# Performance work log

Measured on AMD Instinct MI355X. Metric: run time of the kernel, lower is better.

The kernel has to match this reference:

```python
import jax, jax.numpy as jnp
import numpy as np

B, S, D, H = 4, 2048, 1024, 16
HD = D // H  # head_dim = 64


def setup_inputs() -> dict:
    key = jax.random.key(0)
    ks = jax.random.split(key, 5)
    s = 1.0 / np.sqrt(D)
    return {
        "x": jax.random.normal(ks[0], (B, S, D), jnp.float32),
        "Wq": jax.random.normal(ks[1], (D, D), jnp.float32) * s,
        "Wk": jax.random.normal(ks[2], (D, D), jnp.float32) * s,
        "Wv": jax.random.normal(ks[3], (D, D), jnp.float32) * s,
        "Wo": jax.random.normal(ks[4], (D, D), jnp.float32) * s,
        "bo": jnp.zeros((D,), jnp.float32),
    }


def reference(x, Wq, Wk, Wv, Wo, bo):
    b, s, d = x.shape
    # projections (torch Linear: x @ W.T; weights here stored as [in, out] equivalent)
    q = (x @ Wq).reshape(b, s, H, HD).transpose(0, 2, 1, 3)  # [b,h,s,hd]
    k = (x @ Wk).reshape(b, s, H, HD).transpose(0, 2, 1, 3)
    v = (x @ Wv).reshape(b, s, H, HD).transpose(0, 2, 1, 3)
    scores = jnp.einsum("bhqd,bhkd->bhqk", q, k) * (HD ** -0.5)
    causal = jnp.tril(jnp.ones((s, s), bool))  # mask==0 -> -inf
    scores = jnp.where(causal, scores, -jnp.inf)
    attn = jax.nn.softmax(scores, axis=-1)
    out = jnp.einsum("bhqk,bhkd->bhqd", attn, v)
    out = out.transpose(0, 2, 1, 3).reshape(b, s, d)
    return out @ Wo + bo
```

## Files before the change

kernel.cpp:

```cpp
#include <hip/hip_runtime.h>
#include <cstdint>
#include <cstddef>

typedef __attribute__((ext_vector_type(8))) short bf16x8;
typedef __attribute__((ext_vector_type(4))) short bf16x4;
typedef __attribute__((ext_vector_type(4))) float f32x4;

constexpr int Bsz = 4, Ssz = 2048, Dsz = 1024, Hn = 16, HDsz = 64;
constexpr int Msz = Bsz * Ssz;
constexpr float LOG2E = 1.4426950408889634f;

#define MFMA16(a, b, c) __builtin_amdgcn_mfma_f32_16x16x16bf16_1k(a, b, c, 0, 0, 0)
#define MFMA32(a, b, c) __builtin_amdgcn_mfma_f32_16x16x32_bf16(a, b, c, 0, 0, 0)

__device__ __forceinline__ unsigned short f2bf(float f) {
  union { float f; unsigned int u; } v; v.f = f;
  unsigned int r = v.u + 0x7fffu + ((v.u >> 16) & 1u);
  return (unsigned short)(r >> 16);
}

typedef __attribute__((address_space(1))) const unsigned int gu32;
typedef __attribute__((address_space(3))) unsigned int lu32;
__device__ __forceinline__ void async_cp16(const unsigned short* g, unsigned short* l) {
  __builtin_amdgcn_global_load_lds((gu32*)g, (lu32*)l, 16, 0, 0);
}

__global__ void prep_kernel(const float* __restrict__ x, unsigned short* __restrict__ xb,
                            const float* __restrict__ W0, const float* __restrict__ W1,
                            const float* __restrict__ W2, const float* __restrict__ W3,
                            unsigned short* __restrict__ T0, unsigned short* __restrict__ T1,
                            unsigned short* __restrict__ T2, unsigned short* __restrict__ T3) {
  const int z = blockIdx.z;
  if (z == 4) {
    const int i0 = (blockIdx.y * 32 + blockIdx.x) * 2048 + threadIdx.x;
#pragma unroll
    for (int j = 0; j < 8; j++) {
      const int i = i0 + j * 256;
      const float4 v = reinterpret_cast<const float4*>(x)[i];
      ushort4 o;
      o.x = f2bf(v.x); o.y = f2bf(v.y); o.z = f2bf(v.z); o.w = f2bf(v.w);
      reinterpret_cast<ushort4*>(xb)[i] = o;
    }
    return;
  }
  __shared__ float tile[32][33];
  const float* W = (z == 0) ? W0 : (z == 1) ? W1 : (z == 2) ? W2 : W3;
  unsigned short* Wt = (z == 0) ? T0 : (z == 1) ? T1 : (z == 2) ? T2 : T3;
  int tx = threadIdx.x & 31, ty = threadIdx.x >> 5;
  int bx = blockIdx.x, by = blockIdx.y;
#pragma unroll
  for (int i = 0; i < 4; i++) {
    int k = by * 32 + ty + i * 8;
    tile[ty + i * 8][tx] = W[k * Dsz + bx * 32 + tx];
  }
  __syncthreads();
#pragma unroll
  for (int i = 0; i < 4; i++) {
    int nrow = bx * 32 + ty + i * 8;
    Wt[nrow * Dsz + by * 32 + tx] = f2bf(tile[tx][ty + i * 8]);
  }
}

enum { EPI_QKV = 0, EPI_OUT = 1 };

template <int EPI>
__global__ __launch_bounds__(512, 4)
void gemm_bk64(const unsigned short* __restrict__ A,
               const unsigned short* __restrict__ Bt,
               unsigned short* __restrict__ Qh,
               unsigned short* __restrict__ Kh,
               unsigned short* __restrict__ Vth,
               float* __restrict__ Out,
               const float* __restrict__ bias) {
  __shared__ unsigned short As[128 * 64];
  __shared__ unsigned short Bs[128 * 64];

  const int tid = threadIdx.x;
  const int w = tid >> 6, lane = tid & 63;
  const int l15 = lane & 15, quad = lane >> 4;
  const int wr = w >> 1, wc = w & 1;
  const int orig = blockIdx.y * gridDim.x + blockIdx.x;
  const int xcd = orig & 7, idx = orig >> 3;
  const int bm = (xcd << 3) | (idx & 7);
  const int bn = idx >> 3;
  const int rr = lane >> 3;
  const int scoff = ((lane & 7) ^ rr) * 8;

  f32x4 acc[2][4];
#pragma unroll
  for (int i = 0; i < 2; i++)
#pragma unroll
    for (int j = 0; j < 4; j++) acc[i][j] = (f32x4){0.f, 0.f, 0.f, 0.f};

  const int rowA0 = bm * 128, rowB0 = bn * 128;

  for (int kt = 0; kt < Dsz / 64; kt++) {
#pragma unroll
    for (int i = 0; i < 2; i++) {
      const int r8 = w * 16 + i * 8;
      async_cp16(&A[(size_t)(rowA0 + r8 + rr) * Dsz + kt * 64 + scoff], &As[r8 * 64]);
      async_cp16(&Bt[(size_t)(rowB0 + r8 + rr) * Dsz + kt * 64 + scoff], &Bs[r8 * 64]);
    }
    __syncthreads();

#pragma unroll
    for (int ks = 0; ks < 2; ks++) {
      bf16x8 af[2], bfr[4];
#pragma unroll
      for (int t = 0; t < 2; t++) {
        const int ra = wr * 32 + t * 16 + l15;
        af[t] = *reinterpret_cast<const bf16x8*>(
            &As[ra * 64 + (((ks * 4 + quad) ^ (ra & 7)) * 8)]);
      }
#pragma unroll
      for (int t = 0; t < 4; t++) {
        const int rb = wc * 64 + t * 16 + l15;
        bfr[t] = *reinterpret_cast<const bf16x8*>(
            &Bs[rb * 64 + (((ks * 4 + quad) ^ (rb & 7)) * 8)]);
      }
#pragma unroll
      for (int i = 0; i < 2; i++)
#pragma unroll
        for (int j = 0; j < 4; j++)
          acc[i][j] = MFMA32(af[i], bfr[j], acc[i][j]);
    }
    __syncthreads();
  }

  if (EPI == EPI_QKV) {
    const int proj = (bn * 128) >> 10;
#pragma unroll
    for (int i = 0; i < 2; i++) {
#pragma unroll
      for (int j = 0; j < 4; j++) {
        const int n = bn * 128 + wc * 64 + j * 16 + l15;
        const int nn = n & 1023, h = nn >> 6, hd = nn & 63;
        const int m0 = bm * 128 + wr * 32 + i * 16 + quad * 4;
        const int b = m0 >> 11, s0 = m0 & (Ssz - 1);
        if (proj == 0) {
#pragma unroll
          for (int r = 0; r < 4; r++)
            Qh[((size_t)(b * Hn + h) * Ssz + s0 + r) * HDsz + hd] =
                f2bf(acc[i][j][r] * (0.125f * LOG2E));
        } else if (proj == 1) {
#pragma unroll
          for (int r = 0; r < 4; r++)
            Kh[((size_t)(b * Hn + h) * Ssz + s0 + r) * HDsz + hd] = f2bf(acc[i][j][r]);
        } else {
          ushort4 o;
          o.x = f2bf(acc[i][j][0]); o.y = f2bf(acc[i][j][1]);
          o.z = f2bf(acc[i][j][2]); o.w = f2bf(acc[i][j][3]);
          *reinterpret_cast<ushort4*>(
              &Vth[((size_t)(b * Hn + h) * HDsz + hd) * Ssz + s0]) = o;
        }
      }
    }
  } else {
#pragma unroll
    for (int i = 0; i < 2; i++) {
#pragma unroll
      for (int j = 0; j < 4; j++) {
        const int n = bn * 128 + wc * 64 + j * 16 + l15;
        const int m0 = bm * 128 + wr * 32 + i * 16 + quad * 4;
#pragma unroll
        for (int r = 0; r < 4; r++)
          Out[(size_t)(m0 + r) * Dsz + n] = acc[i][j][r] + bias[n];
      }
    }
  }
}

__global__ __launch_bounds__(256, 4)
void flash_kernel(const unsigned short* __restrict__ Q,
                  const unsigned short* __restrict__ Kg,
                  const unsigned short* __restrict__ Vt,
                  unsigned short* __restrict__ AO) {
  __shared__ unsigned short Ks[64 * 64];
  __shared__ unsigned short Vs[64 * 64];

  const int tid = threadIdx.x;
  const int w = tid >> 6, lane = tid & 63;
  const int l15 = lane & 15, quad = lane >> 4;
  const int rr = lane >> 3;

  const int linear = blockIdx.y * 16 + blockIdx.x;
  const int bh = (linear & 7) * 8 + ((linear >> 3) & 7);
  const int g = linear >> 6, gk = g >> 2, ga = g & 3;
  const int t = (gk == 0) ? 15 - ga : (gk == 1) ? 8 + ga : (gk == 2) ? 7 - ga : ga;

  const unsigned short* Qb = Q + (size_t)bh * Ssz * HDsz;
  const unsigned short* Kb = Kg + (size_t)bh * Ssz * HDsz;
  const unsigned short* Vb = Vt + (size_t)bh * HDsz * Ssz;
  const int b = bh / Hn, h = bh % Hn;

  const int hl = (l15 & 7) ^ ((l15 >> 3) << 2);

  const int q0 = t * 128;
  const int rowStart = q0 + w * 32;

  bf16x8 qf[2][2];
#pragma unroll
  for (int tm = 0; tm < 2; tm++)
#pragma unroll
    for (int ks = 0; ks < 2; ks++)
      qf[tm][ks] = *reinterpret_cast<const bf16x8*>(
          &Qb[(size_t)(rowStart + tm * 16 + l15) * HDsz + ks * 32 + quad * 8]);

  f32x4 oacc[2][4];
  float lpart[2] = {0.f, 0.f};
#pragma unroll
  for (int tm = 0; tm < 2; tm++)
#pragma unroll
    for (int tn = 0; tn < 4; tn++) oacc[tm][tn] = (f32x4){0.f, 0.f, 0.f, 0.f};

  const int nkb = 2 * t + 2;
  for (int kb = 0; kb < nkb; kb++) {
    const int kv0 = kb * 64;
#pragma unroll
    for (int i = 0; i < 2; i++) {
      const int r8 = w * 16 + i * 8;
      const int sc = (((lane & 7) ^ rr ^ (i << 2))) * 8;
      async_cp16(&Kb[(size_t)(kv0 + r8 + rr) * HDsz + sc], &Ks[r8 * 64]);
      async_cp16(&Vb[(size_t)(r8 + rr) * Ssz + kv0 + sc], &Vs[r8 * 64]);
    }
    __syncthreads();

    const bool skip = (kv0 >= rowStart + 32);
    if (!skip) {
      f32x4 sc[4][2];
#pragma unroll
      for (int tn = 0; tn < 4; tn++)
#pragma unroll
        for (int tm = 0; tm < 2; tm++) sc[tn][tm] = (f32x4){0.f, 0.f, 0.f, 0.f};
#pragma unroll
      for (int ks = 0; ks < 2; ks++) {
#pragma unroll
        for (int tn = 0; tn < 4; tn++) {
          const int rk = tn * 16 + l15;
          bf16x8 kf = *reinterpret_cast<const bf16x8*>(
              &Ks[rk * 64 + (((ks * 4 + quad) ^ hl) * 8)]);
#pragma unroll
          for (int tm = 0; tm < 2; tm++)
            sc[tn][tm] = MFMA32(kf, qf[tm][ks], sc[tn][tm]);
        }
      }

      const bool needMask = (kv0 + 63 > rowStart);
      if (needMask) {
#pragma unroll
        for (int tn = 0; tn < 4; tn++)
#pragma unroll
          for (int tm = 0; tm < 2; tm++) {
            const int qrow = rowStart + tm * 16 + l15;
#pragma unroll
            for (int r = 0; r < 4; r++)
              if (kv0 + tn * 16 + quad * 4 + r > qrow) sc[tn][tm][r] = -1e30f;
          }
      }

      unsigned int pk[4][2][2];
#pragma unroll
      for (int tn = 0; tn < 4; tn++)
#pragma unroll
        for (int tm = 0; tm < 2; tm++) {
          union { float f; unsigned int u; } e0, e1, e2, e3;
          e0.f = __builtin_amdgcn_exp2f(sc[tn][tm][0]);
          e1.f = __builtin_amdgcn_exp2f(sc[tn][tm][1]);
          e2.f = __builtin_amdgcn_exp2f(sc[tn][tm][2]);
          e3.f = __builtin_amdgcn_exp2f(sc[tn][tm][3]);
          lpart[tm] += (e0.f + e1.f) + (e2.f + e3.f);
          pk[tn][tm][0] = __builtin_amdgcn_perm(e1.u, e0.u, 0x07060302u);
          pk[tn][tm][1] = __builtin_amdgcn_perm(e3.u, e2.u, 0x07060302u);
        }

#pragma unroll
      for (int tn = 0; tn < 4; tn++) {
        bf16x4 pa[2];
#pragma unroll
        for (int tm = 0; tm < 2; tm++) {
          union { unsigned int u[2]; bf16x4 v; } cv;
          cv.u[0] = pk[tn][tm][0]; cv.u[1] = pk[tn][tm][1];
          pa[tm] = cv.v;
        }
#pragma unroll
        for (int to = 0; to < 4; to++) {
          const int rv = to * 16 + l15;
          const int chunk = tn * 2 + (quad >> 1);
          bf16x4 vf = *reinterpret_cast<const bf16x4*>(
              (const char*)Vs + rv * 128 + ((chunk ^ hl) * 16) + (quad & 1) * 8);
#pragma unroll
          for (int tm = 0; tm < 2; tm++)
            oacc[tm][to] = MFMA16(pa[tm], vf, oacc[tm][to]);
        }
      }
    }
    __syncthreads();
  }

#pragma unroll
  for (int tm = 0; tm < 2; tm++) {
    float lf = lpart[tm];
    lf += __shfl_xor(lf, 16);
    lf += __shfl_xor(lf, 32);
    float linv[4];
#pragma unroll
    for (int r = 0; r < 4; r++) {
      union { float f; int i; } cv;
      cv.f = lf;
      cv.i = __builtin_amdgcn_ds_bpermute((quad * 4 + r) * 4, cv.i);
      linv[r] = 1.f / cv.f;
    }
#pragma unroll
    for (int r = 0; r < 4; r++) {
      const int s = rowStart + tm * 16 + quad * 4 + r;
      const size_t m = (size_t)b * Ssz + s;
#pragma unroll
      for (int tn = 0; tn < 4; tn++) {
        const int n = h * HDsz + tn * 16 + l15;
        AO[m * Dsz + n] = f2bf(oacc[tm][tn][r] * linv[r]);
      }
    }
  }
}

extern "C" void kernel_launch(void* const* d_in, const int* in_sizes, int n_in,
                              void* d_out, int out_size, void* d_ws, size_t ws_size,
                              hipStream_t stream) {
  const float* x  = (const float*)d_in[0];
  const float* Wq = (const float*)d_in[1];
  const float* Wk = (const float*)d_in[2];
  const float* Wv = (const float*)d_in[3];
  const float* Wo = (const float*)d_in[4];
  const float* bo = (const float*)d_in[5];
  float* out = (float*)d_out;

  unsigned short* xb  = (unsigned short*)d_ws;
  unsigned short* Wqt = xb + (size_t)Msz * Dsz;
  unsigned short* Wkt = Wqt + (size_t)Dsz * Dsz;
  unsigned short* Wvt = Wkt + (size_t)Dsz * Dsz;
  unsigned short* Wot = Wvt + (size_t)Dsz * Dsz;
  unsigned short* Qh  = Wot + (size_t)Dsz * Dsz;
  unsigned short* Kh  = Qh + (size_t)Msz * Dsz;
  unsigned short* Vth = Kh + (size_t)Msz * Dsz;
  unsigned short* AO  = Vth + (size_t)Msz * Dsz;

  prep_kernel<<<dim3(32, 32, 5), 256, 0, stream>>>(
      x, xb, Wq, Wk, Wv, Wo, Wqt, Wkt, Wvt, Wot);

  gemm_bk64<EPI_QKV><<<dim3(3 * Dsz / 128, Msz / 128), 512, 0, stream>>>(
      xb, Wqt, Qh, Kh, Vth, nullptr, nullptr);

  flash_kernel<<<dim3(16, Bsz * Hn), 256, 0, stream>>>(Qh, Kh, Vth, AO);

  gemm_bk64<EPI_OUT><<<dim3(Dsz / 128, Msz / 128), 512, 0, stream>>>(
      AO, Wot, nullptr, nullptr, nullptr, out, bo);
}
```

Measured before the change: 225.3 us.

## Halve flash attention query tile to 64 rows and double the grid

The flash kernel now gives each block 64 query rows (16 per wave) instead of 128, launches twice as many blocks, and raises the launch-bounds occupancy hint to 8 blocks per CU. The causal tile schedule is remapped so heavy and light tiles interleave across the 32 query tiles. The aim is more parallelism and a better causal load balance with fewer registers per thread. In exchange, each K/V tile loaded into LDS is reused by half as many query rows, so global and LDS traffic per FLOP roughly doubles.

```diff
diff --git a/kernel.cpp b/kernel.cpp
--- a/kernel.cpp
+++ b/kernel.cpp
@@ -170,7 +170,7 @@
   }
 }
 
-__global__ __launch_bounds__(256, 4)
+__global__ __launch_bounds__(256, 8)
 void flash_kernel(const unsigned short* __restrict__ Q,
                   const unsigned short* __restrict__ Kg,
                   const unsigned short* __restrict__ Vt,
@@ -185,8 +185,9 @@
 
   const int linear = blockIdx.y * 16 + blockIdx.x;
   const int bh = (linear & 7) * 8 + ((linear >> 3) & 7);
-  const int g = linear >> 6, gk = g >> 2, ga = g & 3;
-  const int t = (gk == 0) ? 15 - ga : (gk == 1) ? 8 + ga : (gk == 2) ? 7 - ga : ga;
+  const int g = linear >> 6;
+  const int gk = g >> 2, gr = g & 3;
+  const int t = (gk < 4) ? (gr * 8 + gk) : (31 - (gr * 8 + (gk - 4)));
 
   const unsigned short* Qb = Q + (size_t)bh * Ssz * HDsz;
   const unsigned short* Kb = Kg + (size_t)bh * Ssz * HDsz;
@@ -195,25 +196,21 @@
 
   const int hl = (l15 & 7) ^ ((l15 >> 3) << 2);
 
-  const int q0 = t * 128;
-  const int rowStart = q0 + w * 32;
-
-  bf16x8 qf[2][2];
-#pragma unroll
-  for (int tm = 0; tm < 2; tm++)
-#pragma unroll
-    for (int ks = 0; ks < 2; ks++)
-      qf[tm][ks] = *reinterpret_cast<const bf16x8*>(
-          &Qb[(size_t)(rowStart + tm * 16 + l15) * HDsz + ks * 32 + quad * 8]);
-
-  f32x4 oacc[2][4];
-  float lpart[2] = {0.f, 0.f};
-#pragma unroll
-  for (int tm = 0; tm < 2; tm++)
-#pragma unroll
-    for (int tn = 0; tn < 4; tn++) oacc[tm][tn] = (f32x4){0.f, 0.f, 0.f, 0.f};
-
-  const int nkb = 2 * t + 2;
+  const int q0 = t * 64;
+  const int rowStart = q0 + w * 16;
+
+  bf16x8 qf[2];
+#pragma unroll
+  for (int ks = 0; ks < 2; ks++)
+    qf[ks] = *reinterpret_cast<const bf16x8*>(
+        &Qb[(size_t)(rowStart + l15) * HDsz + ks * 32 + quad * 8]);
+
+  f32x4 oacc[4];
+  float lpart = 0.f;
+#pragma unroll
+  for (int to = 0; to < 4; to++) oacc[to] = (f32x4){0.f, 0.f, 0.f, 0.f};
+
+  const int nkb = t + 1;
   for (int kb = 0; kb < nkb; kb++) {
     const int kv0 = kb * 64;
 #pragma unroll
@@ -225,100 +222,79 @@
     }
     __syncthreads();
 
-    const bool skip = (kv0 >= rowStart + 32);
-    if (!skip) {
-      f32x4 sc[4][2];
+    f32x4 sc[4];
+#pragma unroll
+    for (int tn = 0; tn < 4; tn++) sc[tn] = (f32x4){0.f, 0.f, 0.f, 0.f};
+#pragma unroll
+    for (int ks = 0; ks < 2; ks++) {
+#pragma unroll
+      for (int tn = 0; tn < 4; tn++) {
+        const int rk = tn * 16 + l15;
+        bf16x8 kf = *reinterpret_cast<const bf16x8*>(
+            &Ks[rk * 64 + (((ks * 4 + quad) ^ hl) * 8)]);
+        sc[tn] = MFMA32(kf, qf[ks], sc[tn]);
+      }
+    }
+
+    const bool needMask = (kv0 + 63 > rowStart);
+    if (needMask) {
+      const int qrow = rowStart + l15;
 #pragma unroll
       for (int tn = 0; tn < 4; tn++)
 #pragma unroll
-        for (int tm = 0; tm < 2; tm++) sc[tn][tm] = (f32x4){0.f, 0.f, 0.f, 0.f};
-#pragma unroll
-      for (int ks = 0; ks < 2; ks++) {
-#pragma unroll
-        for (int tn = 0; tn < 4; tn++) {
-          const int rk = tn * 16 + l15;
-          bf16x8 kf = *reinterpret_cast<const bf16x8*>(
-              &Ks[rk * 64 + (((ks * 4 + quad) ^ hl) * 8)]);
-#pragma unroll
-          for (int tm = 0; tm < 2; tm++)
-            sc[tn][tm] = MFMA32(kf, qf[tm][ks], sc[tn][tm]);
-        }
-      }
-
-      const bool needMask = (kv0 + 63 > rowStart);
-      if (needMask) {
-#pragma unroll
-        for (int tn = 0; tn < 4; tn++)
-#pragma unroll
-          for (int tm = 0; tm < 2; tm++) {
-            const int qrow = rowStart + tm * 16 + l15;
-#pragma unroll
-            for (int r = 0; r < 4; r++)
-              if (kv0 + tn * 16 + quad * 4 + r > qrow) sc[tn][tm][r] = -1e30f;
-          }
-      }
-
-      unsigned int pk[4][2][2];
-#pragma unroll
-      for (int tn = 0; tn < 4; tn++)
-#pragma unroll
-        for (int tm = 0; tm < 2; tm++) {
-          union { float f; unsigned int u; } e0, e1, e2, e3;
-          e0.f = __builtin_amdgcn_exp2f(sc[tn][tm][0]);
-          e1.f = __builtin_amdgcn_exp2f(sc[tn][tm][1]);
-          e2.f = __builtin_amdgcn_exp2f(sc[tn][tm][2]);
-          e3.f = __builtin_amdgcn_exp2f(sc[tn][tm][3]);
-          lpart[tm] += (e0.f + e1.f) + (e2.f + e3.f);
-          pk[tn][tm][0] = __builtin_amdgcn_perm(e1.u, e0.u, 0x07060302u);
-          pk[tn][tm][1] = __builtin_amdgcn_perm(e3.u, e2.u, 0x07060302u);
-        }
-
-#pragma unroll
-      for (int tn = 0; tn < 4; tn++) {
-        bf16x4 pa[2];
-#pragma unroll
-        for (int tm = 0; tm < 2; tm++) {
-          union { unsigned int u[2]; bf16x4 v; } cv;
-          cv.u[0] = pk[tn][tm][0]; cv.u[1] = pk[tn][tm][1];
-          pa[tm] = cv.v;
-        }
-#pragma unroll
-        for (int to = 0; to < 4; to++) {
-          const int rv = to * 16 + l15;
-          const int chunk = tn * 2 + (quad >> 1);
-          bf16x4 vf = *reinterpret_cast<const bf16x4*>(
-              (const char*)Vs + rv * 128 + ((chunk ^ hl) * 16) + (quad & 1) * 8);
-#pragma unroll
-          for (int tm = 0; tm < 2; tm++)
-            oacc[tm][to] = MFMA16(pa[tm], vf, oacc[tm][to]);
-        }
+        for (int r = 0; r < 4; r++)
+          if (kv0 + tn * 16 + quad * 4 + r > qrow) sc[tn][r] = -1e30f;
+    }
+
+    unsigned int pk[4][2];
+#pragma unroll
+    for (int tn = 0; tn < 4; tn++) {
+      union { float f; unsigned int u; } e0, e1, e2, e3;
+      e0.f = __builtin_amdgcn_exp2f(sc[tn][0]);
+      e1.f = __builtin_amdgcn_exp2f(sc[tn][1]);
+      e2.f = __builtin_amdgcn_exp2f(sc[tn][2]);
+      e3.f = __builtin_amdgcn_exp2f(sc[tn][3]);
+      lpart += (e0.f + e1.f) + (e2.f + e3.f);
+      pk[tn][0] = __builtin_amdgcn_perm(e1.u, e0.u, 0x07060302u);
+      pk[tn][1] = __builtin_amdgcn_perm(e3.u, e2.u, 0x07060302u);
+    }
+
+#pragma unroll
+    for (int tn = 0; tn < 4; tn++) {
+      union { unsigned int u[2]; bf16x4 v; } cv;
+      cv.u[0] = pk[tn][0]; cv.u[1] = pk[tn][1];
+      const bf16x4 pa = cv.v;
+#pragma unroll
+      for (int to = 0; to < 4; to++) {
+        const int rv = to * 16 + l15;
+        const int chunk = tn * 2 + (quad >> 1);
+        bf16x4 vf = *reinterpret_cast<const bf16x4*>(
+            (const char*)Vs + rv * 128 + ((chunk ^ hl) * 16) + (quad & 1) * 8);
+        oacc[to] = MFMA16(pa, vf, oacc[to]);
       }
     }
     __syncthreads();
   }
 
-#pragma unroll
-  for (int tm = 0; tm < 2; tm++) {
-    float lf = lpart[tm];
-    lf += __shfl_xor(lf, 16);
-    lf += __shfl_xor(lf, 32);
-    float linv[4];
-#pragma unroll
-    for (int r = 0; r < 4; r++) {
-      union { float f; int i; } cv;
-      cv.f = lf;
-      cv.i = __builtin_amdgcn_ds_bpermute((quad * 4 + r) * 4, cv.i);
-      linv[r] = 1.f / cv.f;
-    }
-#pragma unroll
-    for (int r = 0; r < 4; r++) {
-      const int s = rowStart + tm * 16 + quad * 4 + r;
-      const size_t m = (size_t)b * Ssz + s;
-#pragma unroll
-      for (int tn = 0; tn < 4; tn++) {
-        const int n = h * HDsz + tn * 16 + l15;
-        AO[m * Dsz + n] = f2bf(oacc[tm][tn][r] * linv[r]);
-      }
+  float lf = lpart;
+  lf += __shfl_xor(lf, 16);
+  lf += __shfl_xor(lf, 32);
+  float linv[4];
+#pragma unroll
+  for (int r = 0; r < 4; r++) {
+    union { float f; int i; } cv;
+    cv.f = lf;
+    cv.i = __builtin_amdgcn_ds_bpermute((quad * 4 + r) * 4, cv.i);
+    linv[r] = 1.f / cv.f;
+  }
+#pragma unroll
+  for (int r = 0; r < 4; r++) {
+    const int s = rowStart + quad * 4 + r;
+    const size_t m = (size_t)b * Ssz + s;
+#pragma unroll
+    for (int to = 0; to < 4; to++) {
+      const int n = h * HDsz + to * 16 + l15;
+      AO[m * Dsz + n] = f2bf(oacc[to][r] * linv[r]);
     }
   }
 }
@@ -350,7 +326,7 @@
   gemm_bk64<EPI_QKV><<<dim3(3 * Dsz / 128, Msz / 128), 512, 0, stream>>>(
       xb, Wqt, Qh, Kh, Vth, nullptr, nullptr);
 
-  flash_kernel<<<dim3(16, Bsz * Hn), 256, 0, stream>>>(Qh, Kh, Vth, AO);
+  flash_kernel<<<dim3(16, 128), 256, 0, stream>>>(Qh, Kh, Vth, AO);
 
   gemm_bk64<EPI_OUT><<<dim3(Dsz / 128, Msz / 128), 512, 0, stream>>>(
       AO, Wot, nullptr, nullptr, nullptr, out, bo);
```

After: 240.8 us. 1.07x slower.
